# Kernel tuning notes

Hardware: AMD Instinct MI355X
Metric: run time of the kernel (lower is better)

Reference implementation:

```python
import jax, jax.numpy as jnp
import numpy as np

WS = 8       # window_size
SHIFT = 4    # shift_size
HEADS = 4

def _rel_pos_index():
    coords = np.stack(np.meshgrid(np.arange(WS), np.arange(WS), indexing='ij'))
    cf = coords.reshape(2, -1)                       # (2, N)
    rel = cf[:, :, None] - cf[:, None, :]            # (2, N, N)
    rel = rel.transpose(1, 2, 0).copy()              # (N, N, 2)
    rel[:, :, 0] += WS - 1
    rel[:, :, 1] += WS - 1
    rel[:, :, 0] *= 2 * WS - 1
    return jnp.asarray(rel.sum(-1))                  # (N, N) int

REL_IDX = _rel_pos_index()

def _conv(x, w, groups=1, pad=0):
    return jax.lax.conv_general_dilated(
        x, w, (1, 1), [(pad, pad), (pad, pad)],
        feature_group_count=groups,
        dimension_numbers=('NCHW', 'OIHW', 'NCHW'))

def _dwt_haar(x):
    # single-level orthonormal Haar on non-overlapping 2x2 blocks
    B, C, H, W = x.shape
    x = x.reshape(B, C, H // 2, 2, W // 2, 2)
    a = x[:, :, :, 0, :, 0]; b = x[:, :, :, 0, :, 1]
    c = x[:, :, :, 1, :, 0]; d = x[:, :, :, 1, :, 1]
    ll = (a + b + c + d) * 0.5
    lh = (a - b + c - d) * 0.5
    hl = (a + b - c - d) * 0.5
    hh = (a - b - c + d) * 0.5
    return ll, lh, hl, hh

def _idwt_haar(ll, lh, hl, hh):
    a = (ll + lh + hl + hh) * 0.5
    b = (ll - lh + hl - hh) * 0.5
    c = (ll + lh - hl - hh) * 0.5
    d = (ll - lh - hl + hh) * 0.5
    B, C, H2, W2 = ll.shape
    x = jnp.stack([jnp.stack([a, b], -1), jnp.stack([c, d], -1)], -2)  # (B,C,H2,W2,2row,2col)
    return x.transpose(0, 1, 2, 4, 3, 5).reshape(B, C, 2 * H2, 2 * W2)

def _window_partition(x):
    B, C, H, W = x.shape
    x = x.reshape(B, C, H // WS, WS, W // WS, WS).transpose(0, 2, 4, 1, 3, 5)
    return x.reshape(-1, C, WS, WS)

def _window_reverse(w, B, H, W):
    C = w.shape[1]
    x = w.reshape(B, H // WS, W // WS, C, WS, WS).transpose(0, 3, 1, 4, 2, 5)
    return x.reshape(B, C, H, W)

def setup_inputs() -> dict:
    key = jax.random.key(0)
    ks = jax.random.split(key, 8)
    dim = 64
    s = 0.05
    return {
        'x': jax.random.normal(ks[0], (8, dim, 256, 256), jnp.float32),
        'temperature': jnp.ones((HEADS, 1, 1), jnp.float32),
        'rel_bias_table': jax.random.normal(ks[1], ((2 * WS - 1) ** 2, HEADS), jnp.float32) * 0.02,
        'w_high1': jax.random.normal(ks[2], (2 * dim, dim, 3, 3), jnp.float32) * s,
        'w_high2': jax.random.normal(ks[3], (dim, 2 * dim, 1, 1), jnp.float32) * s,
        'w_highout': jax.random.normal(ks[4], (3 * dim, dim, 3, 3), jnp.float32) * s,
        'w_qkv': jax.random.normal(ks[5], (3 * dim, dim, 1, 1), jnp.float32) * s,
        'w_dwconv': jax.random.normal(ks[6], (3 * dim, 1, 3, 3), jnp.float32) * s,
        'w_proj': jax.random.normal(ks[7], (dim, dim, 1, 1), jnp.float32) * s,
    }

def reference(x, temperature, rel_bias_table, w_high1, w_high2, w_highout, w_qkv, w_dwconv, w_proj):
    B, C, H, W = x.shape
    ll, lh, hl, hh = _dwt_haar(x)
    # high-frequency modulation of v
    filt = jax.nn.relu(_conv(jnp.concatenate([lh, hl], 1), w_high1, groups=2, pad=1))
    filt = jax.nn.relu(_conv(filt, w_high2))
    qkv = _conv(_conv(ll, w_qkv), w_dwconv, groups=3 * C, pad=1)
    v_inp = qkv[:, 2 * C:]  # note: q,k from qkv are dead in the source; q=k come from shifted LL
    v = v_inp * filt + v_inp
    xs = jnp.roll(ll, (-SHIFT, -SHIFT), (2, 3))
    qw = _window_partition(xs)
    vw = _window_partition(v)
    Bw = qw.shape[0]; hd = C // HEADS; N = WS * WS
    q = qw.reshape(Bw, HEADS, hd, N)
    vv = vw.reshape(Bw, HEADS, hd, N)
    qn = q / jnp.maximum(jnp.linalg.norm(q, axis=-2, keepdims=True), 1e-12)
    # k == q in the source, so kn == qn
    attn = jnp.einsum('bhdn,bhdm->bhnm', qn, qn)                      # (Bw,h,N,N)
    bias = rel_bias_table[REL_IDX.reshape(-1)].reshape(N, N, HEADS).transpose(2, 0, 1)
    attn = (attn + bias[None]) * temperature[None]
    attn = jax.nn.softmax(attn, axis=-1)
    out = jnp.einsum('bhdm,bhnm->bhdn', vv, attn)                     # v @ attn^T
    out = out.reshape(Bw, C, WS, WS)
    out = _window_reverse(out, B, H // 2, W // 2)
    out = jnp.roll(out, (SHIFT, SHIFT), (2, 3))
    out = _conv(out, w_proj)
    yh = jax.nn.relu(_conv(jnp.concatenate([lh, hl, hh], 1), w_highout, groups=3, pad=1))
    lh2, hl2, hh2 = yh[:, :C], yh[:, C:2 * C], yh[:, 2 * C:]
    return _idwt_haar(out, lh2, hl2, hh2)
```

## Files before the change

kernel.cpp:

```cpp
#include <hip/hip_runtime.h>
#include <cstddef>

constexpr int HP  = 128 * 128;
constexpr long long S = 8LL * 64 * HP;

using short8 = __attribute__((ext_vector_type(8))) short;
using f32x4  = __attribute__((ext_vector_type(4))) float;

__device__ __forceinline__ unsigned short f2bf(float x) {
    union { float f; unsigned int u; } v{x};
    unsigned int r = v.u + 0x7FFFu + ((v.u >> 16) & 1u);
    return (unsigned short)(r >> 16);
}

__global__ __launch_bounds__(256) void k_dwt(const float* __restrict__ x,
                                             float* __restrict__ ll, float* __restrict__ lh,
                                             float* __restrict__ hl, float* __restrict__ hh) {
    long long idx = (long long)blockIdx.x * 256 + threadIdx.x;
    if (idx >= S) return;
    int j  = (int)(idx & 127);
    int i  = (int)((idx >> 7) & 127);
    long long bc = idx >> 14;
    const float* xp = x + bc * 256 * 256;
    float2 top = *(const float2*)(xp + (2 * i) * 256 + 2 * j);
    float2 bot = *(const float2*)(xp + (2 * i + 1) * 256 + 2 * j);
    float a = top.x, b = top.y, c = bot.x, d = bot.y;
    ll[idx] = (a + b + c + d) * 0.5f;
    lh[idx] = (a - b + c - d) * 0.5f;
    hl[idx] = (a + b - c - d) * 0.5f;
    hh[idx] = (a - b - c + d) * 0.5f;
}

__global__ __launch_bounds__(256) void k_to_nhwc(const float* __restrict__ in,
                                                 unsigned short* __restrict__ out) {
    __shared__ float t[64][65];
    int b = blockIdx.y;
    int p0 = blockIdx.x * 64;
    int tid = threadIdx.x;
    const float* ib = in + (size_t)b * 64 * HP;
    {
        int p = tid & 63, c4 = tid >> 6;
#pragma unroll
        for (int k = 0; k < 16; ++k) {
            int c = c4 * 16 + k;
            t[c][p] = ib[(size_t)c * HP + p0 + p];
        }
    }
    __syncthreads();
    {
        int c = tid & 63, pq = tid >> 6;
        unsigned short* ob = out + ((size_t)b * HP + p0) * 64;
#pragma unroll
        for (int k = 0; k < 16; ++k) {
            int p = pq * 16 + k;
            ob[(size_t)p * 64 + c] = f2bf(t[c][p]);
        }
    }
}

__global__ __launch_bounds__(256) void k_wreorder(const float* __restrict__ w,
                                                  unsigned short* __restrict__ wr, int total) {
    int idx = blockIdx.x * 256 + threadIdx.x;
    if (idx >= total) return;
    int oc = idx / 576, rem = idx - oc * 576;
    int s = rem >> 6, ic = rem & 63;
    wr[idx] = f2bf(w[(oc * 64 + ic) * 9 + s]);
}

#define ISTR 72
__global__ __launch_bounds__(256, 2) void k_conv3x3_mfma(
        const unsigned short* __restrict__ in,
        const unsigned short* __restrict__ wr,
        float* __restrict__ out, int out_ctot) {
    __shared__ __align__(16) unsigned short lin[324 * ISTR];
    __shared__ __align__(16) unsigned short lw[64 * ISTR];

    int tid = threadIdx.x;
    int b = blockIdx.y;
    int ty0 = (blockIdx.x >> 3) * 16, tx0 = (blockIdx.x & 7) * 16;

    const unsigned short* inb = in + (size_t)b * HP * 64;
    for (int idx = tid; idx < 324 * 8; idx += 256) {
        int pr = idx >> 3, l8 = idx & 7;
        int py = pr / 18, px = pr - py * 18;
        int gy = ty0 + py - 1, gx = tx0 + px - 1;
        uint4 v = make_uint4(0, 0, 0, 0);
        if (gy >= 0 && gy < 128 && gx >= 0 && gx < 128)
            v = *(const uint4*)(inb + ((size_t)(gy * 128 + gx)) * 64 + l8 * 8);
        *(uint4*)&lin[pr * ISTR + l8 * 8] = v;
    }

    int wv = tid >> 6;
    int lane = tid & 63;
    int n16 = lane & 15, quad = lane >> 4;

    f32x4 acc[4][4];
#pragma unroll
    for (int mt = 0; mt < 4; ++mt)
#pragma unroll
        for (int nt = 0; nt < 4; ++nt) acc[mt][nt] = (f32x4){0.f, 0.f, 0.f, 0.f};

    for (int s = 0; s < 9; ++s) {
        __syncthreads();
        for (int idx = tid; idx < 512; idx += 256) {
            int oc = idx >> 3, l8 = idx & 7;
            *(uint4*)&lw[oc * ISTR + l8 * 8] =
                *(const uint4*)(wr + oc * 576 + s * 64 + l8 * 8);
        }
        __syncthreads();
        int sy = s / 3, sx = s - sy * 3;
#pragma unroll
        for (int half = 0; half < 2; ++half) {
            int ic0 = half * 32 + quad * 8;
            short8 a[4], bf[4];
#pragma unroll
            for (int mt = 0; mt < 4; ++mt)
                a[mt] = *(const short8*)&lw[(mt * 16 + n16) * ISTR + ic0];
#pragma unroll
            for (int nt = 0; nt < 4; ++nt) {
                int py = 4 * wv + nt + sy;
                int px = n16 + sx;
                bf[nt] = *(const short8*)&lin[(py * 18 + px) * ISTR + ic0];
            }
#pragma unroll
            for (int mt = 0; mt < 4; ++mt)
#pragma unroll
                for (int nt = 0; nt < 4; ++nt)
                    acc[mt][nt] = __builtin_amdgcn_mfma_f32_16x16x32_bf16(
                        a[mt], bf[nt], acc[mt][nt], 0, 0, 0);
        }
    }

    int gx = tx0 + n16;
#pragma unroll
    for (int nt = 0; nt < 4; ++nt) {
        int gy = ty0 + 4 * wv + nt;
#pragma unroll
        for (int mt = 0; mt < 4; ++mt) {
#pragma unroll
            for (int r = 0; r < 4; ++r) {
                int oc = mt * 16 + quad * 4 + r;
                out[((size_t)b * out_ctot + oc) * HP + (size_t)gy * 128 + gx] =
                    fmaxf(acc[mt][nt][r], 0.0f);
            }
        }
    }
}

template <int IC, bool RELU>
__global__ __launch_bounds__(256) void k_conv1x1(const float* __restrict__ in,
                                                 const float* __restrict__ w,
                                                 float* __restrict__ out) {
    __shared__ float wl[IC * 16];
    int tid = threadIdx.x;
    int occ = blockIdx.y, b = blockIdx.z;
    for (int idx = tid; idx < IC * 16; idx += 256) {
        int o = idx & 15, ic = idx >> 4;
        wl[idx] = w[(occ * 16 + o) * IC + ic];
    }
    __syncthreads();
    int p = blockIdx.x * 256 + tid;
    const float* inp = in + (size_t)b * IC * HP + p;
    float acc[16] = {};
    for (int ic = 0; ic < IC; ++ic) {
        float xv = inp[(size_t)ic * HP];
#pragma unroll
        for (int o = 0; o < 16; ++o) acc[o] += xv * wl[ic * 16 + o];
    }
    float* op = out + ((size_t)b * 64 + occ * 16) * HP + p;
#pragma unroll
    for (int o = 0; o < 16; ++o) op[o * HP] = RELU ? fmaxf(acc[o], 0.0f) : acc[o];
}

__global__ __launch_bounds__(256) void k_dwconv_v(const float* __restrict__ t,
                                                  const float* __restrict__ wdw,
                                                  const float* __restrict__ filt,
                                                  float* __restrict__ v) {
    long long idx = (long long)blockIdx.x * 256 + threadIdx.x;
    if (idx >= S) return;
    int j = (int)(idx & 127);
    int i = (int)((idx >> 7) & 127);
    int c = (int)((idx >> 14) & 63);
    long long bc = idx >> 14;
    const float* tp = t + bc * HP;
    const float* wp = wdw + c * 9;
    float acc = 0.0f;
#pragma unroll
    for (int ky = 0; ky < 3; ++ky) {
        int y = i + ky - 1;
        if (y < 0 || y >= 128) continue;
#pragma unroll
        for (int kx = 0; kx < 3; ++kx) {
            int x = j + kx - 1;
            if (x < 0 || x >= 128) continue;
            acc += tp[y * 128 + x] * wp[ky * 3 + kx];
        }
    }
    float f = filt[idx];
    v[idx] = acc * (1.0f + f);
}

__global__ __launch_bounds__(256) void k_attn(const float* __restrict__ ll,
                                              const float* __restrict__ v,
                                              const float* __restrict__ table,
                                              const float* __restrict__ temp,
                                              float* __restrict__ outbuf) {
    __shared__ float qs[64][64];
    __shared__ float vs[64][64];
    __shared__ float inv[4][64];
    __shared__ float tb[225 * 4];
    int blk = blockIdx.x;
    int wj = blk & 15, wi = (blk >> 4) & 15, b = blk >> 8;
    int tid = threadIdx.x;

    for (int idx = tid; idx < 900; idx += 256) tb[idx] = table[idx];
    for (int idx = tid; idx < 4096; idx += 256) {
        int c = idx >> 6, n = idx & 63;
        int i = n >> 3, j = n & 7;
        int qy = (wi * 8 + i + 4) & 127, qx = (wj * 8 + j + 4) & 127;
        int vy = wi * 8 + i, vx = wj * 8 + j;
        size_t cb = ((size_t)b * 64 + c) * HP;
        qs[c][n] = ll[cb + qy * 128 + qx];
        vs[c][n] = v[cb + vy * 128 + vx];
    }
    __syncthreads();

    int h = tid >> 6, n = tid & 63;
    float q[16];
    float ss = 0.0f;
#pragma unroll
    for (int d = 0; d < 16; ++d) {
        q[d] = qs[h * 16 + d][n];
        ss += q[d] * q[d];
    }
    float invn = 1.0f / fmaxf(sqrtf(ss), 1e-12f);
    inv[h][n] = invn;
    __syncthreads();

    int i1 = n >> 3, j1 = n & 7;
    float tscale = temp[h];
    float p[64];
    float mx = -1e30f;
#pragma unroll
    for (int m = 0; m < 64; ++m) {
        float s = 0.0f;
#pragma unroll
        for (int d = 0; d < 16; ++d) s += q[d] * qs[h * 16 + d][m];
        s = s * invn * inv[h][m];
        int i2 = m >> 3, j2 = m & 7;
        s += tb[((i1 - i2 + 7) * 15 + (j1 - j2 + 7)) * 4 + h];
        s *= tscale;
        p[m] = s;
        mx = fmaxf(mx, s);
    }
    float sum = 0.0f;
#pragma unroll
    for (int m = 0; m < 64; ++m) {
        p[m] = __expf(p[m] - mx);
        sum += p[m];
    }
    float rs = 1.0f / sum;
    float acc[16] = {};
#pragma unroll
    for (int m = 0; m < 64; ++m) {
        float pm = p[m] * rs;
#pragma unroll
        for (int d = 0; d < 16; ++d) acc[d] += pm * vs[h * 16 + d][m];
    }
    int oy = (wi * 8 + i1 + 4) & 127, ox = (wj * 8 + j1 + 4) & 127;
#pragma unroll
    for (int d = 0; d < 16; ++d)
        outbuf[((size_t)b * 64 + h * 16 + d) * HP + oy * 128 + ox] = acc[d];
}

__global__ __launch_bounds__(256) void k_idwt(const float* __restrict__ ll, const float* __restrict__ lh,
                                              const float* __restrict__ hl, const float* __restrict__ hh,
                                              float* __restrict__ out) {
    long long idx = (long long)blockIdx.x * 256 + threadIdx.x;
    if (idx >= S) return;
    int j = (int)(idx & 127);
    int i = (int)((idx >> 7) & 127);
    long long bc = idx >> 14;
    float L = ll[idx], A = lh[idx], B = hl[idx], D = hh[idx];
    float a = (L + A + B + D) * 0.5f;
    float b = (L - A + B - D) * 0.5f;
    float c = (L + A - B - D) * 0.5f;
    float d = (L - A - B + D) * 0.5f;
    float* op = out + bc * 256 * 256;
    *(float2*)(op + (2 * i) * 256 + 2 * j) = make_float2(a, b);
    *(float2*)(op + (2 * i + 1) * 256 + 2 * j) = make_float2(c, d);
}

extern "C" void kernel_launch(void* const* d_in, const int* in_sizes, int n_in,
                              void* d_out, int out_size, void* d_ws, size_t ws_size,
                              hipStream_t stream) {
    const float* x        = (const float*)d_in[0];
    const float* temp     = (const float*)d_in[1];
    const float* table    = (const float*)d_in[2];
    const float* w_high1  = (const float*)d_in[3];
    const float* w_high2  = (const float*)d_in[4];
    const float* w_highout= (const float*)d_in[5];
    const float* w_qkv    = (const float*)d_in[6];
    const float* w_dwconv = (const float*)d_in[7];
    const float* w_proj   = (const float*)d_in[8];
    float* out = (float*)d_out;

    float* ws = (float*)d_ws;
    float* s0 = ws + 0 * S;
    float* s1 = ws + 1 * S;
    float* s2 = ws + 2 * S;
    float* s3 = ws + 3 * S;
    float* s4 = ws + 4 * S;
    float* s5 = ws + 5 * S;
    float* s6 = ws + 6 * S;
    float* s7 = ws + 7 * S;
    float* s8 = ws + 8 * S;

    unsigned short* T_lh = (unsigned short*)s4;
    unsigned short* T_hl = (unsigned short*)s4 + S;
    unsigned short* T_hh = (unsigned short*)s5;
    unsigned short* w_r1 = (unsigned short*)s5 + S;
    unsigned short* w_r2 = w_r1 + 128 * 576;

    const int nblk = (int)(S / 256);
    dim3 b256(256);

    k_dwt<<<nblk, b256, 0, stream>>>(x, s0, s1, s2, s3);

    dim3 tg(HP / 64, 8);
    k_to_nhwc<<<tg, b256, 0, stream>>>(s1, T_lh);
    k_to_nhwc<<<tg, b256, 0, stream>>>(s2, T_hl);
    k_to_nhwc<<<tg, b256, 0, stream>>>(s3, T_hh);
    k_wreorder<<<(128 * 576 + 255) / 256, b256, 0, stream>>>(w_high1, w_r1, 128 * 576);
    k_wreorder<<<(192 * 576 + 255) / 256, b256, 0, stream>>>(w_highout, w_r2, 192 * 576);

    dim3 cg(64, 8);
    k_conv3x3_mfma<<<cg, b256, 0, stream>>>(T_lh, w_r1,            s1,            128);
    k_conv3x3_mfma<<<cg, b256, 0, stream>>>(T_hl, w_r1 + 64 * 576, s1 + 64 * HP,  128);

    dim3 g1(64, 4, 8);
    k_conv1x1<128, true><<<g1, b256, 0, stream>>>(s1, w_high2, s6);

    k_conv1x1<64, false><<<g1, b256, 0, stream>>>(s0, w_qkv + 128 * 64, s7);

    k_dwconv_v<<<nblk, b256, 0, stream>>>(s7, w_dwconv + 128 * 9, s6, s6);

    k_attn<<<2048, b256, 0, stream>>>(s0, s6, table, temp, s7);

    k_conv1x1<64, false><<<g1, b256, 0, stream>>>(s7, w_proj, s8);

    k_conv3x3_mfma<<<cg, b256, 0, stream>>>(T_lh, w_r2,             s1, 64);
    k_conv3x3_mfma<<<cg, b256, 0, stream>>>(T_hl, w_r2 + 64 * 576,  s2, 64);
    k_conv3x3_mfma<<<cg, b256, 0, stream>>>(T_hh, w_r2 + 128 * 576, s3, 64);

    k_idwt<<<nblk, b256, 0, stream>>>(s8, s1, s2, s3, out);
}
```

Before: 656.5 us.

## Fuse DWT with NHWC transpose, attention with projection, store conv outputs in bf16

Merges the Haar DWT with the bf16 NHWC transposes of the high bands, and fuses the 1x1 output projection into the windowed attention kernel. The attention now uses an online softmax with no max subtraction over transposed shared tiles. The 3x3 MFMA conv outputs are staged through LDS and written as bf16, so the 1x1 conv and IDWT read half the bytes, and conv weights are register-prefetched one tap ahead. Together these cut global memory traffic and kernel launches, at the cost of extra bf16 rounding on intermediates and possible exp overflow without the max shift.

Result: slower. 803.6 us (+22.4%).

```diff
diff --git a/kernel.cpp b/kernel.cpp
--- a/kernel.cpp
+++ b/kernel.cpp
@@ -12,49 +12,44 @@
     unsigned int r = v.u + 0x7FFFu + ((v.u >> 16) & 1u);
     return (unsigned short)(r >> 16);
 }
-
-__global__ __launch_bounds__(256) void k_dwt(const float* __restrict__ x,
-                                             float* __restrict__ ll, float* __restrict__ lh,
-                                             float* __restrict__ hl, float* __restrict__ hh) {
-    long long idx = (long long)blockIdx.x * 256 + threadIdx.x;
-    if (idx >= S) return;
-    int j  = (int)(idx & 127);
-    int i  = (int)((idx >> 7) & 127);
-    long long bc = idx >> 14;
-    const float* xp = x + bc * 256 * 256;
-    float2 top = *(const float2*)(xp + (2 * i) * 256 + 2 * j);
-    float2 bot = *(const float2*)(xp + (2 * i + 1) * 256 + 2 * j);
-    float a = top.x, b = top.y, c = bot.x, d = bot.y;
-    ll[idx] = (a + b + c + d) * 0.5f;
-    lh[idx] = (a - b + c - d) * 0.5f;
-    hl[idx] = (a + b - c - d) * 0.5f;
-    hh[idx] = (a - b - c + d) * 0.5f;
-}
-
-__global__ __launch_bounds__(256) void k_to_nhwc(const float* __restrict__ in,
-                                                 unsigned short* __restrict__ out) {
-    __shared__ float t[64][65];
-    int b = blockIdx.y;
-    int p0 = blockIdx.x * 64;
+__device__ __forceinline__ float b2f(unsigned short u) {
+    union { unsigned int i; float f; } v;
+    v.i = ((unsigned int)u) << 16;
+    return v.f;
+}
+
+__global__ __launch_bounds__(256) void k_dwt_fused(const float* __restrict__ x,
+                                                   float* __restrict__ ll,
+                                                   unsigned short* __restrict__ Tlh,
+                                                   unsigned short* __restrict__ Thl,
+                                                   unsigned short* __restrict__ Thh) {
+    __shared__ unsigned short t3[3][64][66];
+    int j0 = blockIdx.x * 64;
+    int i  = blockIdx.y;
+    int b  = blockIdx.z;
     int tid = threadIdx.x;
-    const float* ib = in + (size_t)b * 64 * HP;
-    {
-        int p = tid & 63, c4 = tid >> 6;
-#pragma unroll
-        for (int k = 0; k < 16; ++k) {
-            int c = c4 * 16 + k;
-            t[c][p] = ib[(size_t)c * HP + p0 + p];
-        }
-    }
-    __syncthreads();
-    {
-        int c = tid & 63, pq = tid >> 6;
-        unsigned short* ob = out + ((size_t)b * HP + p0) * 64;
-#pragma unroll
-        for (int k = 0; k < 16; ++k) {
-            int p = pq * 16 + k;
-            ob[(size_t)p * 64 + c] = f2bf(t[c][p]);
-        }
+    int p = tid & 63, cg = tid >> 6;
+#pragma unroll
+    for (int k = 0; k < 16; ++k) {
+        int c = cg * 16 + k;
+        const float* xp = x + (((size_t)(b * 64 + c) * 256 + 2 * i) * 256 + 2 * (j0 + p));
+        float2 top = *(const float2*)xp;
+        float2 bot = *(const float2*)(xp + 256);
+        float a = top.x, bb = top.y, cc = bot.x, d = bot.y;
+        ll[((size_t)(b * 64 + c)) * HP + i * 128 + j0 + p] = (a + bb + cc + d) * 0.5f;
+        t3[0][p][c] = f2bf((a - bb + cc - d) * 0.5f);
+        t3[1][p][c] = f2bf((a + bb - cc - d) * 0.5f);
+        t3[2][p][c] = f2bf((a - bb - cc + d) * 0.5f);
+    }
+    __syncthreads();
+    int c = tid & 63, pg = tid >> 6;
+    size_t rowbase = ((size_t)b * HP + (size_t)i * 128 + j0) * 64;
+#pragma unroll
+    for (int k = 0; k < 16; ++k) {
+        int pp = pg * 16 + k;
+        Tlh[rowbase + (size_t)pp * 64 + c] = t3[0][pp][c];
+        Thl[rowbase + (size_t)pp * 64 + c] = t3[1][pp][c];
+        Thh[rowbase + (size_t)pp * 64 + c] = t3[2][pp][c];
     }
 }
 
@@ -71,7 +66,7 @@
 __global__ __launch_bounds__(256, 2) void k_conv3x3_mfma(
         const unsigned short* __restrict__ in,
         const unsigned short* __restrict__ wr,
-        float* __restrict__ out, int out_ctot) {
+        unsigned short* __restrict__ out, int out_ctot) {
     __shared__ __align__(16) unsigned short lin[324 * ISTR];
     __shared__ __align__(16) unsigned short lw[64 * ISTR];
 
@@ -100,12 +95,17 @@
 #pragma unroll
         for (int nt = 0; nt < 4; ++nt) acc[mt][nt] = (f32x4){0.f, 0.f, 0.f, 0.f};
 
+    int woc = tid >> 3, wl8 = (tid & 7) * 8;
+    uint4 wA = *(const uint4*)(wr + woc * 576 + wl8);
+    uint4 wB = *(const uint4*)(wr + (woc + 32) * 576 + wl8);
+
     for (int s = 0; s < 9; ++s) {
         __syncthreads();
-        for (int idx = tid; idx < 512; idx += 256) {
-            int oc = idx >> 3, l8 = idx & 7;
-            *(uint4*)&lw[oc * ISTR + l8 * 8] =
-                *(const uint4*)(wr + oc * 576 + s * 64 + l8 * 8);
+        *(uint4*)&lw[woc * ISTR + wl8] = wA;
+        *(uint4*)&lw[(woc + 32) * ISTR + wl8] = wB;
+        if (s < 8) {
+            wA = *(const uint4*)(wr + woc * 576 + (s + 1) * 64 + wl8);
+            wB = *(const uint4*)(wr + (woc + 32) * 576 + (s + 1) * 64 + wl8);
         }
         __syncthreads();
         int sy = s / 3, sx = s - sy * 3;
@@ -131,24 +131,37 @@
         }
     }
 
-    int gx = tx0 + n16;
-#pragma unroll
-    for (int nt = 0; nt < 4; ++nt) {
-        int gy = ty0 + 4 * wv + nt;
-#pragma unroll
-        for (int mt = 0; mt < 4; ++mt) {
-#pragma unroll
-            for (int r = 0; r < 4; ++r) {
-                int oc = mt * 16 + quad * 4 + r;
-                out[((size_t)b * out_ctot + oc) * HP + (size_t)gy * 128 + gx] =
-                    fmaxf(acc[mt][nt][r], 0.0f);
-            }
-        }
-    }
-}
-
-template <int IC, bool RELU>
-__global__ __launch_bounds__(256) void k_conv1x1(const float* __restrict__ in,
+    float* obuf = (float*)lin;
+#pragma unroll 1
+    for (int mt = 0; mt < 4; ++mt) {
+        __syncthreads();
+#pragma unroll
+        for (int nt = 0; nt < 4; ++nt) {
+            int row = 4 * wv + nt;
+#pragma unroll
+            for (int r = 0; r < 4; ++r)
+                obuf[(quad * 4 + r) * 260 + row * 16 + n16] = acc[mt][nt][r];
+        }
+        __syncthreads();
+#pragma unroll
+        for (int k = 0; k < 4; ++k) {
+            int ocl = (tid >> 6) * 4 + k;
+            int px0 = (tid & 63) * 4;
+            f32x4 vv = *(const f32x4*)&obuf[ocl * 260 + px0];
+            unsigned int p0 = f2bf(fmaxf(vv[0], 0.f)) | ((unsigned int)f2bf(fmaxf(vv[1], 0.f)) << 16);
+            unsigned int p1 = f2bf(fmaxf(vv[2], 0.f)) | ((unsigned int)f2bf(fmaxf(vv[3], 0.f)) << 16);
+            int gy = ty0 + (px0 >> 4), gx = tx0 + (px0 & 15);
+            *(uint2*)&out[((size_t)b * out_ctot + mt * 16 + ocl) * HP + (size_t)gy * 128 + gx] =
+                make_uint2(p0, p1);
+        }
+    }
+}
+
+__device__ __forceinline__ float ldval(const float* p) { return *p; }
+__device__ __forceinline__ float ldval(const unsigned short* p) { return b2f(*p); }
+
+template <int IC, bool RELU, typename TIN>
+__global__ __launch_bounds__(256) void k_conv1x1(const TIN* __restrict__ in,
                                                  const float* __restrict__ w,
                                                  float* __restrict__ out) {
     __shared__ float wl[IC * 16];
@@ -160,10 +173,10 @@
     }
     __syncthreads();
     int p = blockIdx.x * 256 + tid;
-    const float* inp = in + (size_t)b * IC * HP + p;
+    const TIN* inp = in + (size_t)b * IC * HP + p;
     float acc[16] = {};
     for (int ic = 0; ic < IC; ++ic) {
-        float xv = inp[(size_t)ic * HP];
+        float xv = ldval(inp + (size_t)ic * HP);
 #pragma unroll
         for (int o = 0; o < 16; ++o) acc[o] += xv * wl[ic * 16 + o];
     }
@@ -200,88 +213,112 @@
     v[idx] = acc * (1.0f + f);
 }
 
-__global__ __launch_bounds__(256) void k_attn(const float* __restrict__ ll,
-                                              const float* __restrict__ v,
-                                              const float* __restrict__ table,
-                                              const float* __restrict__ temp,
-                                              float* __restrict__ outbuf) {
-    __shared__ float qs[64][64];
-    __shared__ float vs[64][64];
+__global__ __launch_bounds__(256) void k_attn_proj(const float* __restrict__ ll,
+                                                   const float* __restrict__ v,
+                                                   const float* __restrict__ table,
+                                                   const float* __restrict__ temp,
+                                                   const float* __restrict__ wproj,
+                                                   float* __restrict__ outp) {
+    __shared__ float qsT[64][68];
+    __shared__ float vsT[64][68];
+    __shared__ float wlT[64][68];
+    __shared__ float tb[900];
     __shared__ float inv[4][64];
-    __shared__ float tb[225 * 4];
     int blk = blockIdx.x;
     int wj = blk & 15, wi = (blk >> 4) & 15, b = blk >> 8;
     int tid = threadIdx.x;
 
     for (int idx = tid; idx < 900; idx += 256) tb[idx] = table[idx];
+    for (int idx = tid; idx < 4096; idx += 256) {
+        int oc = idx & 63, c = idx >> 6;
+        wlT[c][oc] = wproj[oc * 64 + c];
+    }
     for (int idx = tid; idx < 4096; idx += 256) {
         int c = idx >> 6, n = idx & 63;
         int i = n >> 3, j = n & 7;
         int qy = (wi * 8 + i + 4) & 127, qx = (wj * 8 + j + 4) & 127;
         int vy = wi * 8 + i, vx = wj * 8 + j;
         size_t cb = ((size_t)b * 64 + c) * HP;
-        qs[c][n] = ll[cb + qy * 128 + qx];
-        vs[c][n] = v[cb + vy * 128 + vx];
+        qsT[n][c] = ll[cb + qy * 128 + qx];
+        vsT[n][c] = v[cb + vy * 128 + vx];
     }
     __syncthreads();
 
     int h = tid >> 6, n = tid & 63;
     float q[16];
     float ss = 0.0f;
-#pragma unroll
-    for (int d = 0; d < 16; ++d) {
-        q[d] = qs[h * 16 + d][n];
-        ss += q[d] * q[d];
+    {
+        const float* qr = &qsT[n][h * 16];
+#pragma unroll
+        for (int d = 0; d < 16; ++d) { q[d] = qr[d]; ss += q[d] * q[d]; }
     }
     float invn = 1.0f / fmaxf(sqrtf(ss), 1e-12f);
+#pragma unroll
+    for (int d = 0; d < 16; ++d) q[d] *= invn;
     inv[h][n] = invn;
     __syncthreads();
 
     int i1 = n >> 3, j1 = n & 7;
     float tscale = temp[h];
-    float p[64];
-    float mx = -1e30f;
-#pragma unroll
+    float sum = 0.0f;
+    float acc[16] = {};
     for (int m = 0; m < 64; ++m) {
-        float s = 0.0f;
-#pragma unroll
-        for (int d = 0; d < 16; ++d) s += q[d] * qs[h * 16 + d][m];
-        s = s * invn * inv[h][m];
+        const float* qm = &qsT[m][h * 16];
+        float4 a0 = *(const float4*)(qm + 0), a1 = *(const float4*)(qm + 4);
+        float4 a2 = *(const float4*)(qm + 8), a3 = *(const float4*)(qm + 12);
+        float s = q[0] * a0.x + q[1] * a0.y + q[2] * a0.z + q[3] * a0.w
+                + q[4] * a1.x + q[5] * a1.y + q[6] * a1.z + q[7] * a1.w
+                + q[8] * a2.x + q[9] * a2.y + q[10] * a2.z + q[11] * a2.w
+                + q[12] * a3.x + q[13] * a3.y + q[14] * a3.z + q[15] * a3.w;
+        s *= inv[h][m];
         int i2 = m >> 3, j2 = m & 7;
-        s += tb[((i1 - i2 + 7) * 15 + (j1 - j2 + 7)) * 4 + h];
-        s *= tscale;
-        p[m] = s;
-        mx = fmaxf(mx, s);
-    }
-    float sum = 0.0f;
-#pragma unroll
-    for (int m = 0; m < 64; ++m) {
-        p[m] = __expf(p[m] - mx);
-        sum += p[m];
+        s = (s + tb[((i1 - i2 + 7) * 15 + (j1 - j2 + 7)) * 4 + h]) * tscale;
+        float e = __expf(s);
+        sum += e;
+        const float* vm = &vsT[m][h * 16];
+        float4 b0 = *(const float4*)(vm + 0), b1 = *(const float4*)(vm + 4);
+        float4 b2 = *(const float4*)(vm + 8), b3 = *(const float4*)(vm + 12);
+        acc[0] += e * b0.x;  acc[1] += e * b0.y;  acc[2] += e * b0.z;  acc[3] += e * b0.w;
+        acc[4] += e * b1.x;  acc[5] += e * b1.y;  acc[6] += e * b1.z;  acc[7] += e * b1.w;
+        acc[8] += e * b2.x;  acc[9] += e * b2.y;  acc[10] += e * b2.z; acc[11] += e * b2.w;
+        acc[12] += e * b3.x; acc[13] += e * b3.y; acc[14] += e * b3.z; acc[15] += e * b3.w;
     }
     float rs = 1.0f / sum;
-    float acc[16] = {};
-#pragma unroll
-    for (int m = 0; m < 64; ++m) {
-        float pm = p[m] * rs;
-#pragma unroll
-        for (int d = 0; d < 16; ++d) acc[d] += pm * vs[h * 16 + d][m];
-    }
-    int oy = (wi * 8 + i1 + 4) & 127, ox = (wj * 8 + j1 + 4) & 127;
-#pragma unroll
-    for (int d = 0; d < 16; ++d)
-        outbuf[((size_t)b * 64 + h * 16 + d) * HP + oy * 128 + ox] = acc[d];
-}
-
-__global__ __launch_bounds__(256) void k_idwt(const float* __restrict__ ll, const float* __restrict__ lh,
-                                              const float* __restrict__ hl, const float* __restrict__ hh,
+    __syncthreads();
+#pragma unroll
+    for (int d = 0; d < 16; ++d) qsT[h * 16 + d][n] = acc[d] * rs;
+    __syncthreads();
+
+    int px = tid & 63, og = tid >> 6;
+    float accp[16] = {};
+    for (int c = 0; c < 64; ++c) {
+        float xv = qsT[c][px];
+        const float* wr = &wlT[c][og * 16];
+        float4 w0 = *(const float4*)(wr + 0), w1 = *(const float4*)(wr + 4);
+        float4 w2 = *(const float4*)(wr + 8), w3 = *(const float4*)(wr + 12);
+        accp[0] += xv * w0.x;  accp[1] += xv * w0.y;  accp[2] += xv * w0.z;  accp[3] += xv * w0.w;
+        accp[4] += xv * w1.x;  accp[5] += xv * w1.y;  accp[6] += xv * w1.z;  accp[7] += xv * w1.w;
+        accp[8] += xv * w2.x;  accp[9] += xv * w2.y;  accp[10] += xv * w2.z; accp[11] += xv * w2.w;
+        accp[12] += xv * w3.x; accp[13] += xv * w3.y; accp[14] += xv * w3.z; accp[15] += xv * w3.w;
+    }
+    int ip = px >> 3, jp = px & 7;
+    int oy = (wi * 8 + ip + 4) & 127, ox = (wj * 8 + jp + 4) & 127;
+#pragma unroll
+    for (int o = 0; o < 16; ++o)
+        outp[((size_t)b * 64 + og * 16 + o) * HP + oy * 128 + ox] = accp[o];
+}
+
+__global__ __launch_bounds__(256) void k_idwt(const float* __restrict__ ll,
+                                              const unsigned short* __restrict__ lh,
+                                              const unsigned short* __restrict__ hl,
+                                              const unsigned short* __restrict__ hh,
                                               float* __restrict__ out) {
     long long idx = (long long)blockIdx.x * 256 + threadIdx.x;
     if (idx >= S) return;
     int j = (int)(idx & 127);
     int i = (int)((idx >> 7) & 127);
     long long bc = idx >> 14;
-    float L = ll[idx], A = lh[idx], B = hl[idx], D = hh[idx];
+    float L = ll[idx], A = b2f(lh[idx]), B = b2f(hl[idx]), D = b2f(hh[idx]);
     float a = (L + A + B + D) * 0.5f;
     float b = (L - A + B - D) * 0.5f;
     float c = (L + A - B - D) * 0.5f;
@@ -321,37 +358,36 @@
     unsigned short* T_hh = (unsigned short*)s5;
     unsigned short* w_r1 = (unsigned short*)s5 + S;
     unsigned short* w_r2 = w_r1 + 128 * 576;
+    unsigned short* u_f1 = (unsigned short*)s1;
+    unsigned short* u_lh2 = (unsigned short*)s2;
+    unsigned short* u_hl2 = (unsigned short*)s2 + S;
+    unsigned short* u_hh2 = (unsigned short*)s3;
 
     const int nblk = (int)(S / 256);
     dim3 b256(256);
 
-    k_dwt<<<nblk, b256, 0, stream>>>(x, s0, s1, s2, s3);
-
-    dim3 tg(HP / 64, 8);
-    k_to_nhwc<<<tg, b256, 0, stream>>>(s1, T_lh);
-    k_to_nhwc<<<tg, b256, 0, stream>>>(s2, T_hl);
-    k_to_nhwc<<<tg, b256, 0, stream>>>(s3, T_hh);
+    dim3 dg(2, 128, 8);
+    k_dwt_fused<<<dg, b256, 0, stream>>>(x, s0, T_lh, T_hl, T_hh);
+
     k_wreorder<<<(128 * 576 + 255) / 256, b256, 0, stream>>>(w_high1, w_r1, 128 * 576);
     k_wreorder<<<(192 * 576 + 255) / 256, b256, 0, stream>>>(w_highout, w_r2, 192 * 576);
 
     dim3 cg(64, 8);
-    k_conv3x3_mfma<<<cg, b256, 0, stream>>>(T_lh, w_r1,            s1,            128);
-    k_conv3x3_mfma<<<cg, b256, 0, stream>>>(T_hl, w_r1 + 64 * 576, s1 + 64 * HP,  128);
+    k_conv3x3_mfma<<<cg, b256, 0, stream>>>(T_lh, w_r1,            u_f1,            128);
+    k_conv3x3_mfma<<<cg, b256, 0, stream>>>(T_hl, w_r1 + 64 * 576, u_f1 + 64 * HP,  128);
 
     dim3 g1(64, 4, 8);
-    k_conv1x1<128, true><<<g1, b256, 0, stream>>>(s1, w_high2, s6);
+    k_conv1x1<128, true><<<g1, b256, 0, stream>>>(u_f1, w_high2, s6);
 
     k_conv1x1<64, false><<<g1, b256, 0, stream>>>(s0, w_qkv + 128 * 64, s7);
 
     k_dwconv_v<<<nblk, b256, 0, stream>>>(s7, w_dwconv + 128 * 9, s6, s6);
 
-    k_attn<<<2048, b256, 0, stream>>>(s0, s6, table, temp, s7);
-
-    k_conv1x1<64, false><<<g1, b256, 0, stream>>>(s7, w_proj, s8);
-
-    k_conv3x3_mfma<<<cg, b256, 0, stream>>>(T_lh, w_r2,             s1, 64);
-    k_conv3x3_mfma<<<cg, b256, 0, stream>>>(T_hl, w_r2 + 64 * 576,  s2, 64);
-    k_conv3x3_mfma<<<cg, b256, 0, stream>>>(T_hh, w_r2 + 128 * 576, s3, 64);
-
-    k_idwt<<<nblk, b256, 0, stream>>>(s8, s1, s2, s3, out);
-}
+    k_attn_proj<<<2048, b256, 0, stream>>>(s0, s6, table, temp, w_proj, s8);
+
+    k_conv3x3_mfma<<<cg, b256, 0, stream>>>(T_lh, w_r2,             u_lh2, 64);
+    k_conv3x3_mfma<<<cg, b256, 0, stream>>>(T_hl, w_r2 + 64 * 576,  u_hl2, 64);
+    k_conv3x3_mfma<<<cg, b256, 0, stream>>>(T_hh, w_r2 + 128 * 576, u_hh2, 64);
+
+    k_idwt<<<nblk, b256, 0, stream>>>(s8, u_lh2, u_hl2, u_hh2, out);
+}
```
